# Optimization experiments

Hardware: AMD Instinct MI355X
Metric: run time of the kernel (lower is better)

## Reference

```python
import jax, jax.numpy as jnp
import numpy as np

B, H, S, D = 2, 16, 2048, 128
BS = 128  # block_size
NB = S // BS  # num_blocks
SPARSITY_PROB = 0.5


def setup_inputs() -> dict:
    key = jax.random.key(0)
    kq, kk, kv, km = jax.random.split(key, 4)
    query = jax.random.normal(kq, (B, H, S, D), dtype=jnp.float32)
    k_ = jax.random.normal(kk, (B, H, S, D), dtype=jnp.float32)
    v_ = jax.random.normal(kv, (B, H, S, D), dtype=jnp.float32)
    # block pattern: rand < sparsity_prob, diagonal forced True (causal=False)
    block_mask = jax.random.uniform(km, (NB, NB)) < SPARSITY_PROB
    block_mask = block_mask | jnp.eye(NB, dtype=bool)
    return {"query": query, "key": k_, "value": v_,
            "block_mask": block_mask, "block_size": BS}


def reference(query, key, value, block_mask, block_size):
    b, h, s, d = query.shape
    nb = s // block_size
    scale = 1.0 / jnp.sqrt(jnp.float32(d))
    # reshape into blocks: (b, h, nb, bs, d)
    qb = query.reshape(b, h, nb, block_size, d)
    kb = key.reshape(b, h, nb, block_size, d)
    vb = value.reshape(b, h, nb, block_size, d)
    # per-(i,j)-block scores: (b, h, i, j, q, k)
    scores = jnp.einsum('bhiqd,bhjkd->bhijqk', qb, kb) * scale
    # IMPORTANT: softmax is taken independently within each block (axis=-1),
    # matching the original's per-block (non-merged) softmax.
    attn = jax.nn.softmax(scores, axis=-1)
    # zero out inactive blocks, then sum contributions over j
    attn = attn * block_mask[None, None, :, :, None, None].astype(attn.dtype)
    out = jnp.einsum('bhijqk,bhjkd->bhiqd', attn, vb)
    return out.reshape(b, h, s, d)
```

## Files before the change

### kernel.cpp

```cpp
#include <hip/hip_runtime.h>
#include <stdint.h>

#define CBDIM 256
#define WBDIM 256
#define DBDIM 512

#if __has_builtin(__builtin_amdgcn_permlane32_swap) && \
    __has_builtin(__builtin_amdgcn_permlane16_swap)
#define HAVE_PERMLANE_SWAP 1
#else
#define HAVE_PERMLANE_SWAP 0
#endif

typedef __attribute__((ext_vector_type(8))) short short8;
typedef __attribute__((ext_vector_type(4))) float f32x4;

__device__ __forceinline__ unsigned f2bf(float f) {
    union { float f; unsigned u; } a; a.f = f;
    unsigned r = a.u + 0x7fffu + ((a.u >> 16) & 1u);
    return (r >> 16) & 0xffffu;
}
__device__ __forceinline__ unsigned cvtpk_bf16(float a, float b) {
    unsigned r;
    asm("v_cvt_pk_bf16_f32 %0, %1, %2" : "=v"(r) : "v"(a), "v"(b));
    return r;
}
__device__ __forceinline__ float exp2_raw(float x) {
    float r;
    asm("v_exp_f32 %0, %1" : "=v"(r) : "v"(x));
    return r;
}
__device__ __forceinline__ float f4e(float4 v, int e) {
    return e == 0 ? v.x : e == 1 ? v.y : e == 2 ? v.z : v.w;
}
__device__ __forceinline__ unsigned u4e(uint4 v, int e) {
    return e == 0 ? v.x : e == 1 ? v.y : e == 2 ? v.z : v.w;
}
__device__ __forceinline__ uint2 shfl_u2(uint2 v, int src) {
    uint2 r;
    r.x = (unsigned)__shfl((int)v.x, src);
    r.y = (unsigned)__shfl((int)v.y, src);
    return r;
}
__device__ __forceinline__ float xor16_f(float x, int lane) {
#if HAVE_PERMLANE_SWAP
    unsigned u = __float_as_uint(x);
    auto r = __builtin_amdgcn_permlane16_swap(u, u, false, false);
    return __uint_as_float((lane & 16) ? r[0] : r[1]);
#else
    return __shfl_xor(x, 16);
#endif
}
__device__ __forceinline__ float xor32_f(float x, int lane) {
#if HAVE_PERMLANE_SWAP
    unsigned u = __float_as_uint(x);
    auto r = __builtin_amdgcn_permlane32_swap(u, u, false, false);
    return __uint_as_float((lane & 32) ? r[0] : r[1]);
#else
    return __shfl_xor(x, 32);
#endif
}
__device__ __forceinline__ bool detect_bf16(const void* p) {
    unsigned w = ((const unsigned*)p)[threadIdx.x & 63];
    unsigned lo = w & 0xffffu, ex = (lo >> 7) & 0xffu;
    bool pl = (lo == 0u) || (ex >= 0x68u && ex <= 0x86u);
    return __popcll(__ballot(pl)) >= 40;
}
__device__ __forceinline__ void gload_lds16(const void* g, void* l) {
    __builtin_amdgcn_global_load_lds(
        (const __attribute__((address_space(1))) void*)g,
        (__attribute__((address_space(3))) void*)l, 16, 0, 0);
}

__global__ __launch_bounds__(CBDIM)
void convert_fused(const void* __restrict__ Ksrc, const void* __restrict__ Vsrc,
                   uint4* __restrict__ Kw, uint4* __restrict__ Vt,
                   const unsigned char* __restrict__ Mb, int* __restrict__ order,
                   int nIdsK)
{
    const int tid = threadIdx.x;
    const int b = blockIdx.x;
    if (b < 512) {
        bool isBf = detect_bf16(Vsrc);
        if (b == 0 && tid < 64) {
            int tt = tid;
            unsigned mu = ((const unsigned*)Mb)[tt];
            bool maskByte = (__ballot((mu & 0xFFFFFF00u) != 0u) != 0ull);
            int cnt = 0;
            if (tt < 16)
                for (int j = 0; j < 16; ++j) {
                    bool a = maskByte ? (Mb[tt * 16 + j] != 0)
                                      : (((const int*)Mb)[tt * 16 + j] != 0);
                    cnt += a ? 1 : 0;
                }
            int rank = 0;
            for (int j = 0; j < 16; ++j) {
                int cj = __shfl(cnt, j);
                if (cj > cnt || (cj == cnt && j < tt)) ++rank;
            }
            if (tt < 16) order[rank] = tt;
        }
        const size_t kb = (size_t)b * 16384;
        char* base = (char*)(Vt + (size_t)b * 2048);
        auto vaddr = [&](int pp, int d) -> size_t {
            int c = pp >> 1;
            int ks = c >> 2, qd = c & 3;
            int dt = d >> 4, s16 = d & 15;
            return (size_t)((((ks * 8 + dt) * 64 + qd * 16 + s16) << 4)
                            + ((pp & 1) << 3));
        };
#pragma unroll
        for (int it = 0; it < 2; ++it) {
            int id = it * CBDIM + tid, pp = id & 31, dc = id >> 5;
            if (isBf) {
                const unsigned short* vb = (const unsigned short*)Vsrc + kb
                                           + (size_t)(4 * pp) * 128 + dc * 8;
                uint4 r0 = *(const uint4*)(vb);
                uint4 r1 = *(const uint4*)(vb + 128);
                uint4 r2 = *(const uint4*)(vb + 256);
                uint4 r3 = *(const uint4*)(vb + 384);
#pragma unroll
                for (int e = 0; e < 8; ++e) {
                    unsigned h0 = u4e(r0, e >> 1), h1 = u4e(r1, e >> 1);
                    unsigned h2 = u4e(r2, e >> 1), h3 = u4e(r3, e >> 1);
                    if (e & 1) { h0 >>= 16; h1 >>= 16; h2 >>= 16; h3 >>= 16; }
                    uint2 pk;
                    pk.x = (h0 & 0xffffu) | (h1 << 16);
                    pk.y = (h2 & 0xffffu) | (h3 << 16);
                    *(uint2*)(base + vaddr(pp, dc * 8 + e)) = pk;
                }
            } else {
                const float* vb = (const float*)Vsrc + kb
                                  + (size_t)(4 * pp) * 128 + dc * 8;
                float4 ra[4], rb[4];
#pragma unroll
                for (int r = 0; r < 4; ++r) {
                    ra[r] = *(const float4*)(vb + (size_t)r * 128);
                    rb[r] = *(const float4*)(vb + (size_t)r * 128 + 4);
                }
#pragma unroll
                for (int e = 0; e < 8; ++e) {
                    float v0 = (e < 4) ? f4e(ra[0], e) : f4e(rb[0], e - 4);
                    float v1 = (e < 4) ? f4e(ra[1], e) : f4e(rb[1], e - 4);
                    float v2 = (e < 4) ? f4e(ra[2], e) : f4e(rb[2], e - 4);
                    float v3 = (e < 4) ? f4e(ra[3], e) : f4e(rb[3], e - 4);
                    uint2 pk;
                    pk.x = f2bf(v0) | (f2bf(v1) << 16);
                    pk.y = f2bf(v2) | (f2bf(v3) << 16);
                    *(uint2*)(base + vaddr(pp, dc * 8 + e)) = pk;
                }
            }
        }
    } else {
        bool isBf = detect_bf16(Ksrc);
        int stride = ((int)gridDim.x - 512) * CBDIM;
        for (int id = (b - 512) * CBDIM + tid; id < nIdsK; id += stride) {
            int lid = id & 2047, tt = id >> 11;
            int r = lid >> 4, c = (lid & 15) ^ (r & 7);
            size_t eo = (size_t)tt * 16384 + (size_t)r * 128 + c * 8;
            uint4 w;
            if (isBf) {
                w = *(const uint4*)((const unsigned short*)Ksrc + eo);
            } else {
                const float* p = (const float*)Ksrc + eo;
                float4 f0 = *(const float4*)p, f1 = *(const float4*)(p + 4);
                w.x = f2bf(f0.x) | (f2bf(f0.y) << 16);
                w.y = f2bf(f0.z) | (f2bf(f0.w) << 16);
                w.z = f2bf(f1.x) | (f2bf(f1.y) << 16);
                w.w = f2bf(f1.z) | (f2bf(f1.w) << 16);
            }
            Kw[id] = w;
        }
    }
}

template<bool QF32>
__device__ __forceinline__ void attn_core(const void* Qv, const uint4* Kw,
                                          const uint4* Vt, unsigned actm,
                                          void* Ov, char* ldsK, int bh, int i)
{
    constexpr int S = 2048, D = 128;
    const int tid  = threadIdx.x;
    const int lane = tid & 63;
    const int wv   = tid >> 6;
    const int quad = lane >> 4;
    const int l16  = lane & 15;

    const int qb0 = wv * 32;
    const size_t qrowbase = ((size_t)bh * S + (size_t)i * 128) * D;

    short8 qf[2][4];
#pragma unroll
    for (int nt = 0; nt < 2; ++nt) {
        int qrow = qb0 + nt * 16 + l16;
#pragma unroll
        for (int ks = 0; ks < 4; ++ks) {
            int dof = ks * 32 + quad * 8;
            if constexpr (QF32) {
                const float* qp = (const float*)Qv + qrowbase + (size_t)qrow * D + dof;
                float4 f0 = *(const float4*)qp;
                float4 f1 = *(const float4*)(qp + 4);
                short8 v;
                v[0] = (short)f2bf(f0.x); v[1] = (short)f2bf(f0.y);
                v[2] = (short)f2bf(f0.z); v[3] = (short)f2bf(f0.w);
                v[4] = (short)f2bf(f1.x); v[5] = (short)f2bf(f1.y);
                v[6] = (short)f2bf(f1.z); v[7] = (short)f2bf(f1.w);
                qf[nt][ks] = v;
            } else {
                qf[nt][ks] = *(const short8*)((const unsigned short*)Qv
                              + qrowbase + (size_t)qrow * D + dof);
            }
        }
    }

    f32x4 accO[2][8];
#pragma unroll
    for (int a = 0; a < 2; ++a)
#pragma unroll
        for (int b = 0; b < 8; ++b)
            accO[a][b] = (f32x4){0.f, 0.f, 0.f, 0.f};

    const float C2 = 0.08838834764831845f * 1.44269504088896f;

    auto STAGE = [&](const uint4* t, char* lds) {
#pragma unroll
        for (int it = 0; it < 8; ++it) {
            int id = it * WBDIM + tid;
            int lo = (it * WBDIM + wv * 64) * 16;
            gload_lds16(t + id, lds + lo);
        }
        asm volatile("" ::: "memory");
    };
    auto ktile = [&](int jj) { return Kw + (size_t)(bh * 16 + jj) * 2048; };
    auto vtile = [&](int jj) {
        return (const char*)(Vt + (size_t)(bh * 16 + jj) * 2048);
    };

    int j = (int)__builtin_ctz(actm);
    unsigned m = actm & (actm - 1);

    STAGE(ktile(j), ldsK);
    asm volatile("s_waitcnt vmcnt(0)" ::: "memory");
    asm volatile("s_barrier" ::: "memory");
    int cur = 0;

    uint4 vfA[8], vfB[8];

    while (true) {
        int jn = m ? (int)__builtin_ctz(m) : -1;
        if (jn >= 0) m &= m - 1;

        char* kbuf = ldsK + (cur << 15);
        if (jn >= 0) STAGE(ktile(jn), ldsK + ((cur ^ 1) << 15));

        const char* vlane = vtile(j) + (size_t)lane * 16;
#pragma unroll
        for (int dt = 0; dt < 8; ++dt)
            asm volatile("global_load_dwordx4 %0, %1, off"
                         : "=v"(vfA[dt]) : "v"(vlane + dt * 1024));

        f32x4 accS[2][8];
#pragma unroll
        for (int nt = 0; nt < 2; ++nt)
#pragma unroll
            for (int mt = 0; mt < 8; ++mt)
                accS[nt][mt] = (f32x4){0.f, 0.f, 0.f, 0.f};

#pragma unroll
        for (int mt = 0; mt < 8; ++mt) {
            int r = mt * 16 + l16;
            short8 kf[4];
#pragma unroll
            for (int ks = 0; ks < 4; ++ks) {
                int c = ks * 4 + quad;
                kf[ks] = *(const short8*)(kbuf + r * 256 + ((c ^ (r & 7)) << 4));
            }
            __builtin_amdgcn_s_setprio(1);
#pragma unroll
            for (int nt = 0; nt < 2; ++nt)
#pragma unroll
                for (int ks = 0; ks < 4; ++ks)
                    accS[nt][mt] = __builtin_amdgcn_mfma_f32_16x16x32_bf16(
                        kf[ks], qf[nt][ks], accS[nt][mt], 0, 0, 0);
            __builtin_amdgcn_s_setprio(0);
        }

        uint2 p2[2][8];
#pragma unroll
        for (int nt = 0; nt < 2; ++nt) {
            float ps[8];
#pragma unroll
            for (int mt = 0; mt < 8; ++mt) {
                f32x4 p;
#pragma unroll
                for (int rr = 0; rr < 4; ++rr)
                    p[rr] = exp2_raw(accS[nt][mt][rr] * C2);
                accS[nt][mt] = p;
                ps[mt] = (p[0] + p[1]) + (p[2] + p[3]);
            }
            float sum = ((ps[0] + ps[1]) + (ps[2] + ps[3]))
                      + ((ps[4] + ps[5]) + (ps[6] + ps[7]));
            sum += xor16_f(sum, lane);
            sum += xor32_f(sum, lane);
            float rinv = __builtin_amdgcn_rcpf(sum);
#pragma unroll
            for (int mt = 0; mt < 8; ++mt) {
                p2[nt][mt].x = cvtpk_bf16(accS[nt][mt][0] * rinv,
                                          accS[nt][mt][1] * rinv);
                p2[nt][mt].y = cvtpk_bf16(accS[nt][mt][2] * rinv,
                                          accS[nt][mt][3] * rinv);
            }
        }

#pragma unroll
        for (int ks = 0; ks < 4; ++ks) {
            short8 pf[2];
#pragma unroll
            for (int nt = 0; nt < 2; ++nt) {
#if HAVE_PERMLANE_SWAP
                unsigned ax = p2[nt][2 * ks + 0].x, ay = p2[nt][2 * ks + 0].y;
                unsigned bx = p2[nt][2 * ks + 1].x, by = p2[nt][2 * ks + 1].y;
                auto rx = __builtin_amdgcn_permlane32_swap(ax, bx, false, false);
                auto ry = __builtin_amdgcn_permlane32_swap(ay, by, false, false);
                auto sx = __builtin_amdgcn_permlane16_swap(rx[0], rx[1], false, false);
                auto sy = __builtin_amdgcn_permlane16_swap(ry[0], ry[1], false, false);
                union { uint4 u; short8 s; } w;
                w.u.x = sx[0]; w.u.y = sy[0]; w.u.z = sx[1]; w.u.w = sy[1];
                pf[nt] = w.s;
#else
                const int srcA = l16 + ((quad & 1) << 5);
                const int srcB = srcA + 16;
                const bool hiMs = (quad >> 1) != 0;
                uint2 a0 = shfl_u2(p2[nt][2 * ks + 0], srcA);
                uint2 a1 = shfl_u2(p2[nt][2 * ks + 1], srcA);
                uint2 b0 = shfl_u2(p2[nt][2 * ks + 0], srcB);
                uint2 b1 = shfl_u2(p2[nt][2 * ks + 1], srcB);
                uint2 lo, hi;
                lo.x = hiMs ? a1.x : a0.x;  lo.y = hiMs ? a1.y : a0.y;
                hi.x = hiMs ? b1.x : b0.x;  hi.y = hiMs ? b1.y : b0.y;
                union { uint4 u; short8 s; } w;
                w.u.x = lo.x; w.u.y = lo.y; w.u.z = hi.x; w.u.w = hi.y;
                pf[nt] = w.s;
#endif
            }
            if (ks < 3) {
                const char* vb2 = vlane + (ks + 1) * 8192;
#pragma unroll
                for (int dt = 0; dt < 8; ++dt) {
                    if (ks & 1)
                        asm volatile("global_load_dwordx4 %0, %1, off"
                                     : "=v"(vfA[dt]) : "v"(vb2 + dt * 1024));
                    else
                        asm volatile("global_load_dwordx4 %0, %1, off"
                                     : "=v"(vfB[dt]) : "v"(vb2 + dt * 1024));
                }
            }
            if (ks < 3) asm volatile("s_waitcnt vmcnt(8)" ::: "memory");
            else        asm volatile("s_waitcnt vmcnt(0)" ::: "memory");
            __builtin_amdgcn_sched_barrier(0);
            __builtin_amdgcn_s_setprio(1);
#pragma unroll
            for (int dt = 0; dt < 8; ++dt) {
                union { uint4 u; short8 s; } w;
                w.u = (ks & 1) ? vfB[dt] : vfA[dt];
                accO[0][dt] = __builtin_amdgcn_mfma_f32_16x16x32_bf16(
                    pf[0], w.s, accO[0][dt], 0, 0, 0);
                accO[1][dt] = __builtin_amdgcn_mfma_f32_16x16x32_bf16(
                    pf[1], w.s, accO[1][dt], 0, 0, 0);
            }
            __builtin_amdgcn_s_setprio(0);
        }

        if (jn < 0) break;
        asm volatile("s_barrier" ::: "memory");
        cur ^= 1;
        j = jn;
    }

#pragma unroll
    for (int mt = 0; mt < 2; ++mt)
#pragma unroll
        for (int rr = 0; rr < 4; ++rr) {
            int qrow = qb0 + mt * 16 + quad * 4 + rr;
#pragma unroll
            for (int nt = 0; nt < 8; ++nt) {
                size_t idx = qrowbase + (size_t)qrow * D + nt * 16 + l16;
                if constexpr (QF32)
                    ((float*)Ov)[idx] = accO[mt][nt][rr];
                else
                    ((unsigned short*)Ov)[idx] = (unsigned short)f2bf(accO[mt][nt][rr]);
            }
        }
}

__global__ __launch_bounds__(WBDIM, 2)
void attn_ws(const void* __restrict__ Q, const uint4* __restrict__ Kw,
             const uint4* __restrict__ Vt, const unsigned char* __restrict__ Mb,
             const int* __restrict__ order, void* __restrict__ O)
{
    __shared__ uint4 ldsK4[4096];
    int blk = blockIdx.x;
    int bh = ((blk >> 7) << 3) | (blk & 7);
    int slot = (blk >> 3) & 15;
    int i = order[(blk >> 8) ? (15 - slot) : slot];
    bool qBf = detect_bf16(Q);
    unsigned mu = ((const unsigned*)Mb)[threadIdx.x & 63];
    bool maskByte = (__ballot((mu & 0xFFFFFF00u) != 0u) != 0ull);
    unsigned actm = 0;
#pragma unroll
    for (int j = 0; j < 16; ++j) {
        bool a = maskByte ? (Mb[i * 16 + j] != 0)
                          : (((const int*)Mb)[i * 16 + j] != 0);
        actm |= (a ? 1u : 0u) << j;
    }
    if (qBf)
        attn_core<false>(Q, Kw, Vt, actm, O, (char*)ldsK4, bh, i);
    else
        attn_core<true>(Q, Kw, Vt, actm, O, (char*)ldsK4, bh, i);
}

template<bool QF32, bool KVF32>
__device__ __forceinline__ void attn_body(const void* Qv, const void* Kv,
                                          const void* Vv,
                                          const unsigned char* Mb, bool maskByte,
                                          void* Ov, char* ldsK, char* ldsV,
                                          int bh, int i)
{
    constexpr int S = 2048, D = 128;
    const int tid  = threadIdx.x;
    const int lane = tid & 63;
    const int wave = tid >> 6;
    const int quad = lane >> 4;
    const int l16  = lane & 15;

    const int qb0 = wave * 16;
    const size_t qrowbase = ((size_t)bh * S + (size_t)i * 128) * D;

    short8 qf[4];
    {
        int qrow = qb0 + l16;
#pragma unroll
        for (int ks = 0; ks < 4; ++ks) {
            int dof = ks * 32 + quad * 8;
            if constexpr (QF32) {
                const float* qp = (const float*)Qv + qrowbase + (size_t)qrow * D + dof;
                float4 f0 = *(const float4*)qp;
                float4 f1 = *(const float4*)(qp + 4);
                short8 v;
                v[0] = (short)f2bf(f0.x); v[1] = (short)f2bf(f0.y);
                v[2] = (short)f2bf(f0.z); v[3] = (short)f2bf(f0.w);
                v[4] = (short)f2bf(f1.x); v[5] = (short)f2bf(f1.y);
                v[6] = (short)f2bf(f1.z); v[7] = (short)f2bf(f1.w);
                qf[ks] = v;
            } else {
                qf[ks] = *(const short8*)((const unsigned short*)Qv
                          + qrowbase + (size_t)qrow * D + dof);
            }
        }
    }

    f32x4 accO[8];
#pragma unroll
    for (int b = 0; b < 8; ++b)
        accO[b] = (f32x4){0.f, 0.f, 0.f, 0.f};

    const float C2 = 0.08838834764831845f * 1.44269504088896f;
    const int srcA = l16 + ((quad & 1) << 5);
    const int srcB = srcA + 16;
    const bool hiMs = (quad >> 1) != 0;

    for (int j = 0; j < 16; ++j) {
        bool active = maskByte ? (Mb[i * 16 + j] != 0)
                               : (((const int*)Mb)[i * 16 + j] != 0);
        if (!active) continue;

        __syncthreads();
        const size_t kb = ((size_t)bh * S + (size_t)j * 128) * D;

        if constexpr (KVF32) {
#pragma unroll
            for (int it = 0; it < 8; ++it) {
                int f = it * DBDIM + tid;
                int r = f >> 5, c4 = f & 31;
                float4 v = ((const float4*)((const float*)Kv + kb))[f];
                uint2 pk;
                pk.x = f2bf(v.x) | (f2bf(v.y) << 16);
                pk.y = f2bf(v.z) | (f2bf(v.w) << 16);
                int ch = c4 >> 1;
                *(uint2*)(ldsK + r * 256 + ((ch ^ (r & 7)) << 4)
                          + ((c4 & 1) << 3)) = pk;
            }
        } else {
#pragma unroll
            for (int it = 0; it < 4; ++it) {
                int id = it * DBDIM + tid;
                int r = id >> 4, ch = id & 15;
                uint4 v = ((const uint4*)((const unsigned short*)Kv + kb))[id];
                *(uint4*)(ldsK + r * 256 + ((ch ^ (r & 7)) << 4)) = v;
            }
        }

        {
            int id = tid, pp = id & 31, dc = id >> 5;
            if constexpr (KVF32) {
                const float* vb = (const float*)Vv + kb + (size_t)(4 * pp) * D + dc * 8;
                float4 ra[4], rb[4];
#pragma unroll
                for (int r = 0; r < 4; ++r) {
                    ra[r] = *(const float4*)(vb + (size_t)r * D);
                    rb[r] = *(const float4*)(vb + (size_t)r * D + 4);
                }
#pragma unroll
                for (int e = 0; e < 8; ++e) {
                    float v0 = (e < 4) ? f4e(ra[0], e) : f4e(rb[0], e - 4);
                    float v1 = (e < 4) ? f4e(ra[1], e) : f4e(rb[1], e - 4);
                    float v2 = (e < 4) ? f4e(ra[2], e) : f4e(rb[2], e - 4);
                    float v3 = (e < 4) ? f4e(ra[3], e) : f4e(rb[3], e - 4);
                    uint2 pk;
                    pk.x = f2bf(v0) | (f2bf(v1) << 16);
                    pk.y = f2bf(v2) | (f2bf(v3) << 16);
                    int d = dc * 8 + e;
                    *(uint2*)(ldsV + d * 256 + (((pp >> 1) ^ (d & 7)) << 4)
                              + ((pp & 1) << 3)) = pk;
                }
            } else {
                const unsigned short* vb = (const unsigned short*)Vv + kb
                                           + (size_t)(4 * pp) * D + dc * 8;
                uint4 r0 = *(const uint4*)(vb);
                uint4 r1 = *(const uint4*)(vb + D);
                uint4 r2 = *(const uint4*)(vb + 2 * D);
                uint4 r3 = *(const uint4*)(vb + 3 * D);
#pragma unroll
                for (int e = 0; e < 8; ++e) {
                    unsigned h0 = u4e(r0, e >> 1), h1 = u4e(r1, e >> 1);
                    unsigned h2 = u4e(r2, e >> 1), h3 = u4e(r3, e >> 1);
                    if (e & 1) { h0 >>= 16; h1 >>= 16; h2 >>= 16; h3 >>= 16; }
                    uint2 pk;
                    pk.x = (h0 & 0xffffu) | (h1 << 16);
                    pk.y = (h2 & 0xffffu) | (h3 << 16);
                    int d = dc * 8 + e;
                    *(uint2*)(ldsV + d * 256 + (((pp >> 1) ^ (d & 7)) << 4)
                              + ((pp & 1) << 3)) = pk;
                }
            }
        }
        __syncthreads();

        f32x4 accS[8];
#pragma unroll
        for (int mt = 0; mt < 8; ++mt)
            accS[mt] = (f32x4){0.f, 0.f, 0.f, 0.f};

#pragma unroll
        for (int mt = 0; mt < 8; ++mt) {
            int r = mt * 16 + l16;
            short8 kf[4];
#pragma unroll
            for (int ks = 0; ks < 4; ++ks) {
                int c = ks * 4 + quad;
                kf[ks] = *(const short8*)(ldsK + r * 256 + ((c ^ (r & 7)) << 4));
            }
#pragma unroll
            for (int ks = 0; ks < 4; ++ks)
                accS[mt] = __builtin_amdgcn_mfma_f32_16x16x32_bf16(
                    kf[ks], qf[ks], accS[mt], 0, 0, 0);
        }

        float ps[8];
#pragma unroll
        for (int mt = 0; mt < 8; ++mt) {
            f32x4 p;
#pragma unroll
            for (int rr = 0; rr < 4; ++rr)
                p[rr] = exp2f(accS[mt][rr] * C2);
            accS[mt] = p;
            ps[mt] = (p[0] + p[1]) + (p[2] + p[3]);
        }
        float sum = ((ps[0] + ps[1]) + (ps[2] + ps[3]))
                  + ((ps[4] + ps[5]) + (ps[6] + ps[7]));
        sum += __shfl_xor(sum, 16);
        sum += __shfl_xor(sum, 32);
        float rinv = 1.0f / sum;

        uint2 p2[8];
#pragma unroll
        for (int mt = 0; mt < 8; ++mt) {
            p2[mt].x = f2bf(accS[mt][0] * rinv) | (f2bf(accS[mt][1] * rinv) << 16);
            p2[mt].y = f2bf(accS[mt][2] * rinv) | (f2bf(accS[mt][3] * rinv) << 16);
        }

#pragma unroll
        for (int ks = 0; ks < 4; ++ks) {
            short8 pf;
            {
                uint2 a0 = shfl_u2(p2[2 * ks + 0], srcA);
                uint2 a1 = shfl_u2(p2[2 * ks + 1], srcA);
                uint2 b0 = shfl_u2(p2[2 * ks + 0], srcB);
                uint2 b1 = shfl_u2(p2[2 * ks + 1], srcB);
                uint2 lo, hi;
                lo.x = hiMs ? a1.x : a0.x;  lo.y = hiMs ? a1.y : a0.y;
                hi.x = hiMs ? b1.x : b0.x;  hi.y = hiMs ? b1.y : b0.y;
                union { uint4 u; short8 s; } w;
                w.u.x = lo.x; w.u.y = lo.y; w.u.z = hi.x; w.u.w = hi.y;
                pf = w.s;
            }
#pragma unroll
            for (int dt = 0; dt < 8; ++dt) {
                int d = dt * 16 + l16;
                int c = ks * 4 + quad;
                short8 vf = *(const short8*)(ldsV + d * 256 + ((c ^ (d & 7)) << 4));
                accO[dt] = __builtin_amdgcn_mfma_f32_16x16x32_bf16(
                    pf, vf, accO[dt], 0, 0, 0);
            }
        }
    }

#pragma unroll
    for (int rr = 0; rr < 4; ++rr) {
        int qrow = qb0 + quad * 4 + rr;
#pragma unroll
        for (int dt = 0; dt < 8; ++dt) {
            size_t idx = qrowbase + (size_t)qrow * D + dt * 16 + l16;
            if constexpr (QF32)
                ((float*)Ov)[idx] = accO[dt][rr];
            else
                ((unsigned short*)Ov)[idx] = (unsigned short)f2bf(accO[dt][rr]);
        }
    }
}

__global__ __launch_bounds__(DBDIM, 4)
void attn_direct(const void* __restrict__ Q, const void* __restrict__ K,
                 const void* __restrict__ V,
                 const unsigned char* __restrict__ Mb, void* __restrict__ O)
{
    __shared__ uint4 ldsK4[2048];
    __shared__ uint4 ldsV4[2048];
    int blk = blockIdx.x;
    int bh = ((blk >> 7) << 3) | (blk & 7);
    int i  = (blk >> 3) & 15;
    bool qBf = detect_bf16(Q);
    unsigned mu = ((const unsigned*)Mb)[threadIdx.x & 63];
    bool maskByte = (__ballot((mu & 0xFFFFFF00u) != 0u) != 0ull);
    if (qBf)
        attn_body<false, false>(Q, K, V, Mb, maskByte, O,
                                (char*)ldsK4, (char*)ldsV4, bh, i);
    else
        attn_body<true, true>(Q, K, V, Mb, maskByte, O,
                              (char*)ldsK4, (char*)ldsV4, bh, i);
}

extern "C" void kernel_launch(void* const* d_in, const int* in_sizes, int n_in,
                              void* d_out, int out_size, void* d_ws, size_t ws_size,
                              hipStream_t stream) {
    const int NIDS = 512 * 2048;
    const size_t need = (size_t)NIDS * 16 * 2 + 256;
    if (ws_size >= need) {
        uint4* Kw = (uint4*)d_ws;
        uint4* Vt = Kw + NIDS;
        int* order = (int*)(Vt + NIDS);
        convert_fused<<<1536, CBDIM, 0, stream>>>(d_in[1], d_in[2], Kw, Vt,
                                                  (const unsigned char*)d_in[3],
                                                  order, NIDS);
        attn_ws<<<512, WBDIM, 0, stream>>>(d_in[0], Kw, Vt,
                                           (const unsigned char*)d_in[3],
                                           order, d_out);
    } else {
        attn_direct<<<512, DBDIM, 0, stream>>>(d_in[0], d_in[1], d_in[2],
                                               (const unsigned char*)d_in[3], d_out);
    }
}
```

Before: 189.0 us.

## Split attention block across 8 waves with 16 query rows each

```diff
diff --git a/kernel.cpp b/kernel.cpp
--- a/kernel.cpp
+++ b/kernel.cpp
@@ -2,7 +2,7 @@
 #include <stdint.h>
 
 #define CBDIM 256
-#define WBDIM 256
+#define ABDIM 512
 #define DBDIM 512
 
 #if __has_builtin(__builtin_amdgcn_permlane32_swap) && \
@@ -186,13 +186,12 @@
     const int quad = lane >> 4;
     const int l16  = lane & 15;
 
-    const int qb0 = wv * 32;
+    const int qb0 = wv * 16;
     const size_t qrowbase = ((size_t)bh * S + (size_t)i * 128) * D;
 
-    short8 qf[2][4];
-#pragma unroll
-    for (int nt = 0; nt < 2; ++nt) {
-        int qrow = qb0 + nt * 16 + l16;
+    short8 qf[4];
+    {
+        int qrow = qb0 + l16;
 #pragma unroll
         for (int ks = 0; ks < 4; ++ks) {
             int dof = ks * 32 + quad * 8;
@@ -205,28 +204,26 @@
                 v[2] = (short)f2bf(f0.z); v[3] = (short)f2bf(f0.w);
                 v[4] = (short)f2bf(f1.x); v[5] = (short)f2bf(f1.y);
                 v[6] = (short)f2bf(f1.z); v[7] = (short)f2bf(f1.w);
-                qf[nt][ks] = v;
+                qf[ks] = v;
             } else {
-                qf[nt][ks] = *(const short8*)((const unsigned short*)Qv
-                              + qrowbase + (size_t)qrow * D + dof);
-            }
-        }
-    }
-
-    f32x4 accO[2][8];
-#pragma unroll
-    for (int a = 0; a < 2; ++a)
-#pragma unroll
-        for (int b = 0; b < 8; ++b)
-            accO[a][b] = (f32x4){0.f, 0.f, 0.f, 0.f};
+                qf[ks] = *(const short8*)((const unsigned short*)Qv
+                          + qrowbase + (size_t)qrow * D + dof);
+            }
+        }
+    }
+
+    f32x4 accO[8];
+#pragma unroll
+    for (int b = 0; b < 8; ++b)
+        accO[b] = (f32x4){0.f, 0.f, 0.f, 0.f};
 
     const float C2 = 0.08838834764831845f * 1.44269504088896f;
 
     auto STAGE = [&](const uint4* t, char* lds) {
 #pragma unroll
-        for (int it = 0; it < 8; ++it) {
-            int id = it * WBDIM + tid;
-            int lo = (it * WBDIM + wv * 64) * 16;
+        for (int it = 0; it < 4; ++it) {
+            int id = it * ABDIM + tid;
+            int lo = (it * ABDIM + wv * 64) * 16;
             gload_lds16(t + id, lds + lo);
         }
         asm volatile("" ::: "memory");
@@ -244,7 +241,7 @@
     asm volatile("s_barrier" ::: "memory");
     int cur = 0;
 
-    uint4 vfA[8], vfB[8];
+    uint4 vf[8];
 
     while (true) {
         int jn = m ? (int)__builtin_ctz(m) : -1;
@@ -253,18 +250,10 @@
         char* kbuf = ldsK + (cur << 15);
         if (jn >= 0) STAGE(ktile(jn), ldsK + ((cur ^ 1) << 15));
 
-        const char* vlane = vtile(j) + (size_t)lane * 16;
-#pragma unroll
-        for (int dt = 0; dt < 8; ++dt)
-            asm volatile("global_load_dwordx4 %0, %1, off"
-                         : "=v"(vfA[dt]) : "v"(vlane + dt * 1024));
-
-        f32x4 accS[2][8];
-#pragma unroll
-        for (int nt = 0; nt < 2; ++nt)
-#pragma unroll
-            for (int mt = 0; mt < 8; ++mt)
-                accS[nt][mt] = (f32x4){0.f, 0.f, 0.f, 0.f};
+        f32x4 accS[8];
+#pragma unroll
+        for (int mt = 0; mt < 8; ++mt)
+            accS[mt] = (f32x4){0.f, 0.f, 0.f, 0.f};
 
 #pragma unroll
         for (int mt = 0; mt < 8; ++mt) {
@@ -277,98 +266,89 @@
             }
             __builtin_amdgcn_s_setprio(1);
 #pragma unroll
-            for (int nt = 0; nt < 2; ++nt)
-#pragma unroll
-                for (int ks = 0; ks < 4; ++ks)
-                    accS[nt][mt] = __builtin_amdgcn_mfma_f32_16x16x32_bf16(
-                        kf[ks], qf[nt][ks], accS[nt][mt], 0, 0, 0);
+            for (int ks = 0; ks < 4; ++ks)
+                accS[mt] = __builtin_amdgcn_mfma_f32_16x16x32_bf16(
+                    kf[ks], qf[ks], accS[mt], 0, 0, 0);
             __builtin_amdgcn_s_setprio(0);
         }
 
-        uint2 p2[2][8];
-#pragma unroll
-        for (int nt = 0; nt < 2; ++nt) {
-            float ps[8];
-#pragma unroll
-            for (int mt = 0; mt < 8; ++mt) {
-                f32x4 p;
-#pragma unroll
-                for (int rr = 0; rr < 4; ++rr)
-                    p[rr] = exp2_raw(accS[nt][mt][rr] * C2);
-                accS[nt][mt] = p;
-                ps[mt] = (p[0] + p[1]) + (p[2] + p[3]);
-            }
-            float sum = ((ps[0] + ps[1]) + (ps[2] + ps[3]))
-                      + ((ps[4] + ps[5]) + (ps[6] + ps[7]));
-            sum += xor16_f(sum, lane);
-            sum += xor32_f(sum, lane);
-            float rinv = __builtin_amdgcn_rcpf(sum);
-#pragma unroll
-            for (int mt = 0; mt < 8; ++mt) {
-                p2[nt][mt].x = cvtpk_bf16(accS[nt][mt][0] * rinv,
-                                          accS[nt][mt][1] * rinv);
-                p2[nt][mt].y = cvtpk_bf16(accS[nt][mt][2] * rinv,
-                                          accS[nt][mt][3] * rinv);
-            }
+        const char* vlane = vtile(j) + (size_t)lane * 16;
+#pragma unroll
+        for (int dt = 0; dt < 8; ++dt)
+            asm volatile("global_load_dwordx4 %0, %1, off"
+                         : "=v"(vf[dt]) : "v"(vlane + dt * 1024));
+
+        float ps[8];
+#pragma unroll
+        for (int mt = 0; mt < 8; ++mt) {
+            f32x4 p;
+#pragma unroll
+            for (int rr = 0; rr < 4; ++rr)
+                p[rr] = exp2_raw(accS[mt][rr] * C2);
+            accS[mt] = p;
+            ps[mt] = (p[0] + p[1]) + (p[2] + p[3]);
+        }
+        float sum = ((ps[0] + ps[1]) + (ps[2] + ps[3]))
+                  + ((ps[4] + ps[5]) + (ps[6] + ps[7]));
+        sum += xor16_f(sum, lane);
+        sum += xor32_f(sum, lane);
+        float rinv = __builtin_amdgcn_rcpf(sum);
+
+        uint2 p2[8];
+#pragma unroll
+        for (int mt = 0; mt < 8; ++mt) {
+            p2[mt].x = cvtpk_bf16(accS[mt][0] * rinv, accS[mt][1] * rinv);
+            p2[mt].y = cvtpk_bf16(accS[mt][2] * rinv, accS[mt][3] * rinv);
         }
 
 #pragma unroll
         for (int ks = 0; ks < 4; ++ks) {
-            short8 pf[2];
-#pragma unroll
-            for (int nt = 0; nt < 2; ++nt) {
+            short8 pf;
+            {
 #if HAVE_PERMLANE_SWAP
-                unsigned ax = p2[nt][2 * ks + 0].x, ay = p2[nt][2 * ks + 0].y;
-                unsigned bx = p2[nt][2 * ks + 1].x, by = p2[nt][2 * ks + 1].y;
+                unsigned ax = p2[2 * ks + 0].x, ay = p2[2 * ks + 0].y;
+                unsigned bx = p2[2 * ks + 1].x, by = p2[2 * ks + 1].y;
                 auto rx = __builtin_amdgcn_permlane32_swap(ax, bx, false, false);
                 auto ry = __builtin_amdgcn_permlane32_swap(ay, by, false, false);
                 auto sx = __builtin_amdgcn_permlane16_swap(rx[0], rx[1], false, false);
                 auto sy = __builtin_amdgcn_permlane16_swap(ry[0], ry[1], false, false);
                 union { uint4 u; short8 s; } w;
                 w.u.x = sx[0]; w.u.y = sy[0]; w.u.z = sx[1]; w.u.w = sy[1];
-                pf[nt] = w.s;
+                pf = w.s;
 #else
                 const int srcA = l16 + ((quad & 1) << 5);
                 const int srcB = srcA + 16;
                 const bool hiMs = (quad >> 1) != 0;
-                uint2 a0 = shfl_u2(p2[nt][2 * ks + 0], srcA);
-                uint2 a1 = shfl_u2(p2[nt][2 * ks + 1], srcA);
-                uint2 b0 = shfl_u2(p2[nt][2 * ks + 0], srcB);
-                uint2 b1 = shfl_u2(p2[nt][2 * ks + 1], srcB);
+                uint2 a0 = shfl_u2(p2[2 * ks + 0], srcA);
+                uint2 a1 = shfl_u2(p2[2 * ks + 1], srcA);
+                uint2 b0 = shfl_u2(p2[2 * ks + 0], srcB);
+                uint2 b1 = shfl_u2(p2[2 * ks + 1], srcB);
                 uint2 lo, hi;
                 lo.x = hiMs ? a1.x : a0.x;  lo.y = hiMs ? a1.y : a0.y;
                 hi.x = hiMs ? b1.x : b0.x;  hi.y = hiMs ? b1.y : b0.y;
                 union { uint4 u; short8 s; } w;
                 w.u.x = lo.x; w.u.y = lo.y; w.u.z = hi.x; w.u.w = hi.y;
-                pf[nt] = w.s;
+                pf = w.s;
 #endif
             }
+            asm volatile("s_waitcnt vmcnt(0)" ::: "memory");
+            __builtin_amdgcn_sched_barrier(0);
+            __builtin_amdgcn_s_setprio(1);
+#pragma unroll
+            for (int dt = 0; dt < 8; ++dt) {
+                union { uint4 u; short8 s; } w;
+                w.u = vf[dt];
+                accO[dt] = __builtin_amdgcn_mfma_f32_16x16x32_bf16(
+                    pf, w.s, accO[dt], 0, 0, 0);
+            }
+            __builtin_amdgcn_s_setprio(0);
             if (ks < 3) {
                 const char* vb2 = vlane + (ks + 1) * 8192;
 #pragma unroll
-                for (int dt = 0; dt < 8; ++dt) {
-                    if (ks & 1)
-                        asm volatile("global_load_dwordx4 %0, %1, off"
-                                     : "=v"(vfA[dt]) : "v"(vb2 + dt * 1024));
-                    else
-                        asm volatile("global_load_dwordx4 %0, %1, off"
-                                     : "=v"(vfB[dt]) : "v"(vb2 + dt * 1024));
-                }
-            }
-            if (ks < 3) asm volatile("s_waitcnt vmcnt(8)" ::: "memory");
-            else        asm volatile("s_waitcnt vmcnt(0)" ::: "memory");
-            __builtin_amdgcn_sched_barrier(0);
-            __builtin_amdgcn_s_setprio(1);
-#pragma unroll
-            for (int dt = 0; dt < 8; ++dt) {
-                union { uint4 u; short8 s; } w;
-                w.u = (ks & 1) ? vfB[dt] : vfA[dt];
-                accO[0][dt] = __builtin_amdgcn_mfma_f32_16x16x32_bf16(
-                    pf[0], w.s, accO[0][dt], 0, 0, 0);
-                accO[1][dt] = __builtin_amdgcn_mfma_f32_16x16x32_bf16(
-                    pf[1], w.s, accO[1][dt], 0, 0, 0);
-            }
-            __builtin_amdgcn_s_setprio(0);
+                for (int dt = 0; dt < 8; ++dt)
+                    asm volatile("global_load_dwordx4 %0, %1, off"
+                                 : "=v"(vf[dt]) : "v"(vb2 + dt * 1024));
+            }
         }
 
         if (jn < 0) break;
@@ -378,22 +358,20 @@
     }
 
 #pragma unroll
-    for (int mt = 0; mt < 2; ++mt)
-#pragma unroll
-        for (int rr = 0; rr < 4; ++rr) {
-            int qrow = qb0 + mt * 16 + quad * 4 + rr;
-#pragma unroll
-            for (int nt = 0; nt < 8; ++nt) {
-                size_t idx = qrowbase + (size_t)qrow * D + nt * 16 + l16;
-                if constexpr (QF32)
-                    ((float*)Ov)[idx] = accO[mt][nt][rr];
-                else
-                    ((unsigned short*)Ov)[idx] = (unsigned short)f2bf(accO[mt][nt][rr]);
-            }
-        }
-}
-
-__global__ __launch_bounds__(WBDIM, 2)
+    for (int rr = 0; rr < 4; ++rr) {
+        int qrow = qb0 + quad * 4 + rr;
+#pragma unroll
+        for (int dt = 0; dt < 8; ++dt) {
+            size_t idx = qrowbase + (size_t)qrow * D + dt * 16 + l16;
+            if constexpr (QF32)
+                ((float*)Ov)[idx] = accO[dt][rr];
+            else
+                ((unsigned short*)Ov)[idx] = (unsigned short)f2bf(accO[dt][rr]);
+        }
+    }
+}
+
+__global__ __launch_bounds__(ABDIM, 2)
 void attn_ws(const void* __restrict__ Q, const uint4* __restrict__ Kw,
              const uint4* __restrict__ Vt, const unsigned char* __restrict__ Mb,
              const int* __restrict__ order, void* __restrict__ O)
@@ -662,7 +640,7 @@
         convert_fused<<<1536, CBDIM, 0, stream>>>(d_in[1], d_in[2], Kw, Vt,
                                                   (const unsigned char*)d_in[3],
                                                   order, NIDS);
-        attn_ws<<<512, WBDIM, 0, stream>>>(d_in[0], Kw, Vt,
+        attn_ws<<<512, ABDIM, 0, stream>>>(d_in[0], Kw, Vt,
                                            (const unsigned char*)d_in[3],
                                            order, d_out);
     } else {
```

Result: slower. 228.4 us (+20.8%).
